# Performance work log

Measured on AMD Instinct MI355X. Metric: run time of the kernel, lower is better.

The kernel has to match this reference:

```python
import jax, jax.numpy as jnp
import numpy as np

D, R, C = 4, 6, 32
P = 2 * R + 1          # 13 (both pixel patch and memory patch, since memory_patch_R == R)
N = P * P              # 169
DIL_INT = 15


def corr_sampler(f1, f2, p, dil):
    """SpatialCorrelationSampler(kernel_size=1, patch_size=p, dilation_patch=dil).
    out[b,i,j,y,x] = sum_c f1[b,c,y,x] * f2[b,c, y+(i-Rp)*dil, x+(j-Rp)*dil] (zero pad)."""
    Rp = (p - 1) // 2
    pad = Rp * dil
    b, c, h, w = f1.shape
    f2p = jnp.pad(f2, ((0, 0), (0, 0), (pad, pad), (pad, pad)))
    outs = [jnp.einsum('bchw,bchw->bhw', f1, f2p[:, :, i * dil:i * dil + h, j * dil:j * dil + w])
            for i in range(p) for j in range(p)]
    return jnp.stack(outs, 1).reshape(b, p, p, h, w)


def bilinear_gather(im, ys, xs):
    """Bilinear sample im [b,c,H,W] at float coords ys,xs [b,N,h,w]; zeros outside."""
    H, W = im.shape[2], im.shape[3]
    y0 = jnp.floor(ys)
    x0 = jnp.floor(xs)
    wy = ys - y0
    wx = xs - x0

    def g(yi, xi):
        valid = ((yi >= 0) & (yi < H) & (xi >= 0) & (xi < W)).astype(im.dtype)
        yc = jnp.clip(yi, 0, H - 1).astype(jnp.int32)
        xc = jnp.clip(xi, 0, W - 1).astype(jnp.int32)
        out = jax.vmap(lambda imb, yb, xb: imb[:, yb, xb])(im, yc, xc)  # [b,c,N,h,w]
        return out * valid[:, None]

    return (g(y0, x0) * ((1 - wy) * (1 - wx))[:, None]
            + g(y0, x0 + 1) * ((1 - wy) * wx)[:, None]
            + g(y0 + 1, x0) * (wy * (1 - wx))[:, None]
            + g(y0 + 1, x0 + 1) * (wy * wx)[:, None])


def deform_im2col(im, offset, p):
    """Deformable im2col: for each output pixel (y,x) and kernel pos (ky,kx),
    bilinearly sample im at (y+ky-Rp+off_y, x+kx-Rp+off_x). offset [...,0]=x, [...,1]=y.
    Returns [b,c,p*p,h,w]."""
    b, c, h, w = im.shape
    Rp = (p - 1) // 2
    ky, kx = jnp.meshgrid(jnp.arange(p) - Rp, jnp.arange(p) - Rp, indexing='ij')
    ky = ky.reshape(-1).astype(im.dtype)
    kx = kx.reshape(-1).astype(im.dtype)
    ys = (jnp.arange(h, dtype=im.dtype)[None, None, :, None]
          + ky[None, :, None, None] + offset[..., 1][:, None])  # [b,N,h,w]
    xs = (jnp.arange(w, dtype=im.dtype)[None, None, None, :]
          + kx[None, :, None, None] + offset[..., 0][:, None])
    return bilinear_gather(im, ys, xs)


def unfold_patches(x, p, pad):
    """F.unfold(kernel_size=p, padding=pad) -> [b,c,p*p,h,w]."""
    b, c, h, w = x.shape
    xp = jnp.pad(x, ((0, 0), (0, 0), (pad, pad), (pad, pad)))
    cols = [xp[:, :, i:i + h, j:j + w] for i in range(p) for j in range(p)]
    return jnp.stack(cols, 2)


def _forward(feats_r, feats_t, quantized_r, ref_index, current_ind):
    ri = np.asarray(ref_index)
    ci = int(current_ind)
    diffs = [ci - int(x) for x in ri]
    nsearch = sum(1 for d in diffs if d > DIL_INT)
    dirates = [min(4, d // DIL_INT + 1) for d in diffs if d > DIL_INT]
    nref = feats_r.shape[0]
    b, c, h, w = feats_t.shape

    # offset grid: _y,_x = meshgrid(ij) so grid[...,0]=x-offset, grid[...,1]=y-offset
    _y, _x = jnp.meshgrid(jnp.arange(-R, R + 1), jnp.arange(-R, R + 1), indexing='ij')
    grid = jnp.stack([_x, _y], -1).astype(feats_t.dtype)  # [P,P,2]

    corrs_pixel = []
    offset0 = []
    for s in range(nsearch):
        cc = corr_sampler(feats_t, feats_r[s], P, dirates[s])             # [b,P,P,h,w]
        soft = jax.nn.softmax(cc.reshape(b, N, h * w), axis=1).reshape(b, P, P, h, w)
        off = jnp.einsum('bijhw,ijd->bhwd', soft, grid) * dirates[s]      # [b,h,w,2]
        offset0.append(off)
        col0 = deform_im2col(feats_r[s], off, P)                          # [b,c,N,h,w]
        corrs_pixel.append(jnp.einsum('bchw,bcnhw->bnhw', feats_t, col0).reshape(b, N, h * w))
    for ind in range(nsearch, nref):
        corrs_pixel.append(corr_sampler(feats_t, feats_r[ind], P, 1).reshape(b, N, h * w))

    corr_pixel = jax.nn.softmax(jnp.concatenate(corrs_pixel, 1), axis=1)  # [b,nref*N,h*w]

    # prep: float + stride-D subsampling (C-channel input, so no one-hot branch)
    qr = [quantized_r[i][:, :, ::D, ::D] for i in range(nref)]            # [b,C,h,w]
    cols = [deform_im2col(qr[i], offset0[i], P).reshape(b, C, N, h * w) for i in range(nsearch)]
    cols += [unfold_patches(qr[i], P, R).reshape(b, C, N, h * w) for i in range(nsearch, nref)]
    image_uf = jnp.concatenate(cols, 2)                                   # [b,C,nref*N,h*w]

    out = jnp.einsum('bkl,bckl->bcl', corr_pixel, image_uf).reshape(b, C, h, w)
    return out


def setup_inputs() -> dict:
    key = jax.random.key(0)
    k1, k2, k3 = jax.random.split(key, 3)
    feats_r = jax.random.normal(k1, (3, 1, 64, 56, 56), jnp.float32) * 0.2
    feats_t = jax.random.normal(k2, (1, 64, 56, 56), jnp.float32) * 0.2
    quantized_r = jax.random.uniform(k3, (3, 1, 32, 224, 224), jnp.float32)
    return {
        'feats_r': feats_r,
        'feats_t': feats_t,
        'quantized_r': quantized_r,
        'ref_index': np.array([0, 30, 39], dtype=np.int64),
        'current_ind': 40,
    }


def reference(feats_r, feats_t, quantized_r, ref_index, current_ind):
    return _forward(feats_r, feats_t, quantized_r, ref_index, current_ind)
```

## Files before the change

kernel.cpp:

```cpp
#include <hip/hip_runtime.h>

#define HW    56
#define NPIX  3136
#define CH    64
#define CQ    32
#define PS    13
#define NPOS  169
#define GS    14
#define NG    196
#define G1    15
#define NG1   225

typedef __attribute__((ext_vector_type(8))) short short8;
typedef __attribute__((ext_vector_type(8))) ushort ushort8;
typedef __attribute__((ext_vector_type(4))) float f32x4;

__device__ inline ushort f2bf(float f) {
  unsigned u = __float_as_uint(f);
  return (ushort)((u + 0x7fffu + ((u >> 16) & 1u)) >> 16);
}
__device__ inline float bf2f(ushort u) {
  return __uint_as_float((unsigned)u << 16);
}
__device__ inline void wave_sync() {
  asm volatile("s_waitcnt lgkmcnt(0)" ::: "memory");
  __builtin_amdgcn_sched_barrier(0);
}

__global__ __launch_bounds__(256) void prep_all(
    const float* __restrict__ ft_in,
    const float* __restrict__ fr_in,
    const float* __restrict__ q_in,
    ushort* __restrict__ ft_out,
    ushort* __restrict__ fr_out,
    ushort* __restrict__ qout,
    float* __restrict__ zrow) {
  __shared__ float smem[CQ * (HW + 1)];
  int bid = blockIdx.x, tid = threadIdx.x;
  if (bid < 784) {
    if (bid == 0 && tid < 64) zrow[tid] = 0.f;
    int m = bid / 196, t = bid - m * 196;
    int row0 = (t / 98) * 32;
    int col0 = (t - (t / 98) * 98) * 32;
    const float* src = (m == 0) ? ft_in : fr_in + (size_t)(m - 1) * CH * NPIX;
    ushort* dst      = (m == 0) ? ft_out : fr_out + (size_t)(m - 1) * NPIX * CH;
    int ty = tid >> 3, tx4 = (tid & 7) * 4;
    f32x4 v = *(const f32x4*)&src[(size_t)(row0 + ty) * NPIX + col0 + tx4];
    *(f32x4*)&smem[ty * 33 + tx4] = v;
    __syncthreads();
    int px = tid >> 3, c4 = (tid & 7) * 4;
    ushort4 o;
    o.x = f2bf(smem[(c4 + 0) * 33 + px]);
    o.y = f2bf(smem[(c4 + 1) * 33 + px]);
    o.z = f2bf(smem[(c4 + 2) * 33 + px]);
    o.w = f2bf(smem[(c4 + 3) * 33 + px]);
    *(ushort4*)&dst[(size_t)(col0 + px) * CH + row0 + c4] = o;
  } else {
    int q = bid - 784;
    int r = q / HW, yy = q - r * HW;
    for (int idx = tid; idx < CQ * HW; idx += 256) {
      int c = idx / HW, xx = idx - c * HW;
      smem[c * (HW + 1) + xx] = q_in[((size_t)(r * CQ + c) * 224 + yy * 4) * 224 + xx * 4];
    }
    __syncthreads();
    for (int idx = tid; idx < CQ * HW; idx += 256) {
      int xx = idx >> 5, c = idx & 31;
      qout[(size_t)r * NPIX * CQ + (size_t)(yy * HW + xx) * CQ + c] = f2bf(smem[c * (HW + 1) + xx]);
    }
  }
}

__global__ __launch_bounds__(256, 4) void colorizer_main(
    const ushort* __restrict__ ftb,
    const ushort* __restrict__ frb,
    const ushort* __restrict__ qrb,
    const ushort* __restrict__ zrow,
    float* __restrict__ out)
{
  __shared__ float C1[1024];
  __shared__ float C2[1024];
  __shared__ int   pw[4 * 832];
  __shared__ float s12w[16];
  __shared__ float Sas[4];
  __shared__ float fqr0[128];
  __shared__ float red2[512];

  int tid = threadIdx.x;
  int wid = tid >> 6, lane = tid & 63;
  int mrow = lane & 15, klane = lane >> 4;

  int bx = blockIdx.x % 28, by = blockIdx.x / 28;
  int Y0 = by * 2, X0 = bx * 2;
  int dy = wid >> 1, dx = wid & 1;
  int y = Y0 + dy, x = X0 + dx;
  int pix = y * HW + x;

  int*   wb   = pw + wid * 832;
  float* e    = (float*)wb;
  float* D    = (float*)(wb + 176);
  float* wg   = (float*)(wb + 384);
  int*   offg = wb + 608;
  float* cc   = (float*)offg;

  if (lane < 16) offg[208 + lane] = -1;

  const ushort* frb0 = frb;
  const ushort* frb1 = frb + (size_t)NPIX * CH;
  const ushort* frb2 = frb + (size_t)2 * NPIX * CH;
  const ushort* qr0b = qrb;
  const ushort* qr1b = qrb + (size_t)NPIX * CQ;
  const ushort* qr2b = qrb + (size_t)2 * NPIX * CQ;

  const ushort* fb = ftb + (size_t)pix * CH;
  const ushort* plo = (mrow == 0) ? (fb + klane * 8) : zrow;
  const ushort* phi = (mrow == 0) ? (fb + 32 + klane * 8) : zrow;
  short8 b_lo = *(const short8*)plo;
  short8 b_hi = *(const short8*)phi;

  const ushort* fb4 = (mrow < 4)
      ? (ftb + (size_t)((Y0 + (mrow >> 1)) * HW + X0 + (mrow & 1)) * CH)
      : zrow;
  short8 b4_lo = *(const short8*)(fb4 + klane * 8);
  short8 b4_hi = *(const short8*)(fb4 + 32 + klane * 8);

#pragma unroll
  for (int k = 0; k < 11; ++k) {
    if (k < 8) {
      int j = wid + 4 * k;
      if (j < 30) {
        int r = (j >= 15);
        int t = j - r * 15;
        int g = t * 16 + mrow;
        int gy = g / G1, gx = g - gy * G1;
        int sy = Y0 - 6 + gy, sx = X0 - 6 + gx;
        bool v = (g < NG1) && ((unsigned)sy < HW) && ((unsigned)sx < HW);
        const ushort* base = r ? frb2 : frb1;
        const ushort* rb = v ? (base + (size_t)(sy * HW + sx) * CH) : zrow;
        short8 alo = *(const short8*)(rb + klane * 8);
        short8 ahi = *(const short8*)(rb + 32 + klane * 8);
        f32x4 acc = {0.f, 0.f, 0.f, 0.f};
        acc = __builtin_amdgcn_mfma_f32_16x16x32_bf16(alo, b4_lo, acc, 0, 0, 0);
        acc = __builtin_amdgcn_mfma_f32_16x16x32_bf16(ahi, b4_hi, acc, 0, 0, 0);
        int col = lane & 15;
        if (col < 4) {
          float* Cd = r ? C2 : C1;
          int row0 = t * 16 + (lane >> 4) * 4;
#pragma unroll
          for (int q = 0; q < 4; ++q) Cd[(row0 + q) * 4 + col] = acc[q];
        }
      }
    }
    {
      int d = k * 16 + mrow;
      int ii = d / PS, jj = d - ii * PS;
      int sy = y + (ii - 6) * 3, sx = x + (jj - 6) * 3;
      bool v = (d < NPOS) && ((unsigned)sy < HW) && ((unsigned)sx < HW);
      const ushort* rb = v ? (frb0 + (size_t)(sy * HW + sx) * CH) : zrow;
      short8 alo = *(const short8*)(rb + klane * 8);
      short8 ahi = *(const short8*)(rb + 32 + klane * 8);
      f32x4 acc = {0.f, 0.f, 0.f, 0.f};
      acc = __builtin_amdgcn_mfma_f32_16x16x32_bf16(alo, b_lo, acc, 0, 0, 0);
      acc = __builtin_amdgcn_mfma_f32_16x16x32_bf16(ahi, b_hi, acc, 0, 0, 0);
      if (mrow == 0) *(f32x4*)&cc[k * 16 + klane * 4] = acc;
    }
  }
  __syncthreads();

  float sacc = 0.f;
#pragma unroll
  for (int t = 0; t < 8; ++t) {
    int idx = tid + t * 256;
    int ref = idx >> 10;
    int ix = idx & 1023;
    int g = ix >> 2, p = ix & 3;
    int gy = g / G1, gx = g - gy * G1;
    int ii = gy - (p >> 1), jj = gx - (p & 1);
    bool win = (g < NG1) && ((unsigned)ii < PS) && ((unsigned)jj < PS);
    float* Cd = ref ? C2 : C1;
    float val = Cd[ix];
    float ev = win ? __expf(val) : 0.f;
    Cd[ix] = ev;
    sacc += ev;
  }
#pragma unroll
  for (int o = 4; o <= 32; o <<= 1) sacc += __shfl_xor(sacc, o);
  if (lane < 4) s12w[wid * 4 + lane] = sacc;

  float se = 0.f, sxe = 0.f, sye = 0.f;
#pragma unroll
  for (int k = 0; k < 3; ++k) {
    int id = lane + 64 * k;
    if (id < NPOS) {
      float ex = __expf(cc[id]);
      int pi = id / PS, pj = id - (id / PS) * PS;
      se += ex;
      sxe += ex * (float)(pj - 6);
      sye += ex * (float)(pi - 6);
    }
  }
#pragma unroll
  for (int o = 1; o < 64; o <<= 1) {
    se  += __shfl_xor(se, o);
    sxe += __shfl_xor(sxe, o);
    sye += __shfl_xor(sye, o);
  }
  float offx = 3.f * sxe / se;
  float offy = 3.f * sye / se;

  float fy0 = floorf(offy), fx0 = floorf(offx);
  int   iy0 = (int)fy0,     ix0 = (int)fx0;
  float wyf = offy - fy0,   wxf = offx - fx0;
  float w00 = (1.f - wyf) * (1.f - wxf), w01 = (1.f - wyf) * wxf;
  float w10 = wyf * (1.f - wxf),         w11 = wyf * wxf;
  __syncthreads();

  {
    int q8 = tid & 7, s = tid >> 3;
    float a12[4][4];
#pragma unroll
    for (int p = 0; p < 4; ++p)
#pragma unroll
      for (int c = 0; c < 4; ++c) a12[p][c] = 0.f;
#pragma unroll
    for (int i = 0; i < 8; ++i) {
      int g = s + 32 * i;
      if (g < NG1) {
        int gy = g / G1, gx = g - gy * G1;
        int sy = Y0 - 6 + gy, sx = X0 - 6 + gx;
        if (((unsigned)sy < HW) && ((unsigned)sx < HW)) {
          size_t ro = (size_t)(sy * HW + sx) * CQ + q8 * 4;
          ushort4 u1 = *(const ushort4*)(qr1b + ro);
          ushort4 u2 = *(const ushort4*)(qr2b + ro);
          f32x4 w1 = *(f32x4*)&C1[g * 4];
          f32x4 w2 = *(f32x4*)&C2[g * 4];
          float q1[4] = {bf2f(u1.x), bf2f(u1.y), bf2f(u1.z), bf2f(u1.w)};
          float q2[4] = {bf2f(u2.x), bf2f(u2.y), bf2f(u2.z), bf2f(u2.w)};
#pragma unroll
          for (int p = 0; p < 4; ++p)
#pragma unroll
            for (int c = 0; c < 4; ++c)
              a12[p][c] += w1[p] * q1[c] + w2[p] * q2[c];
        }
      }
    }
#pragma unroll
    for (int o = 8; o <= 32; o <<= 1)
#pragma unroll
      for (int p = 0; p < 4; ++p)
#pragma unroll
        for (int c = 0; c < 4; ++c)
          a12[p][c] += __shfl_xor(a12[p][c], o);
    if (lane < 8) {
#pragma unroll
      for (int p = 0; p < 4; ++p)
#pragma unroll
        for (int c = 0; c < 4; ++c)
          red2[wid * 128 + lane * 16 + p * 4 + c] = a12[p][c];
    }
  }

#pragma unroll
  for (int g = 0; g < 13; ++g) {
    int d = g * 16 + mrow;
    int a = d / GS, bq = d - a * GS;
    int sy = y + iy0 + a - 6, sx = x + ix0 + bq - 6;
    bool vA = (d < NG) && ((unsigned)sy < HW) && ((unsigned)sx < HW);
    int roA = sy * HW + sx;
    const ushort* rbA = vA ? (frb0 + (size_t)roA * CH) : zrow;
    short8 aAlo = *(const short8*)(rbA + klane * 8);
    short8 aAhi = *(const short8*)(rbA + 32 + klane * 8);
    f32x4 accA = {0.f, 0.f, 0.f, 0.f};
    accA = __builtin_amdgcn_mfma_f32_16x16x32_bf16(aAlo, b_lo, accA, 0, 0, 0);
    accA = __builtin_amdgcn_mfma_f32_16x16x32_bf16(aAhi, b_hi, accA, 0, 0, 0);
    if (klane == 0) offg[d] = vA ? roA : -1;
    if (mrow == 0) *(f32x4*)&D[g * 16 + klane * 4] = accA;
  }
  wave_sync();

  float ps = 0.f;
#pragma unroll
  for (int k = 0; k < 3; ++k) {
    int id = lane + 64 * k;
    if (id < NPOS) {
      int pi = id / PS, pj = id - (id / PS) * PS;
      float c0 = w00 * D[pi * GS + pj]       + w01 * D[pi * GS + pj + 1]
               + w10 * D[(pi + 1) * GS + pj] + w11 * D[(pi + 1) * GS + pj + 1];
      float ex = __expf(c0);
      e[id] = ex;
      ps += ex;
    } else if (id < 176) {
      e[id] = 0.f;
    }
  }
#pragma unroll
  for (int o = 1; o < 64; o <<= 1) ps += __shfl_xor(ps, o);
  if (lane == 0)
    Sas[wid] = ps + s12w[wid] + s12w[4 + wid] + s12w[8 + wid] + s12w[12 + wid];
  wave_sync();

#pragma unroll
  for (int k = 0; k < 4; ++k) {
    int t = lane + 64 * k;
    if (t < 224) {
      float acc = 0.f;
      if (t < NG) {
        int a = t / GS, bq2 = t - (t / GS) * GS;
        if (a < PS && bq2 < PS) acc += w00 * e[a * PS + bq2];
        if (a < PS && bq2 >= 1) acc += w01 * e[a * PS + bq2 - 1];
        if (a >= 1 && bq2 < PS) acc += w10 * e[(a - 1) * PS + bq2];
        if (a >= 1 && bq2 >= 1) acc += w11 * e[(a - 1) * PS + bq2 - 1];
      }
      wg[t] = acc;
    }
  }
  wave_sync();

  int slot = lane >> 2, ln4 = lane & 3;
  float acc8[8];
#pragma unroll
  for (int c = 0; c < 8; ++c) acc8[c] = 0.f;
#pragma unroll
  for (int k = 0; k < 14; ++k) {
    int d = slot + k * 16;
    int ro = offg[d];
    if (ro >= 0) {
      float w = wg[d];
      ushort8 u = *(const ushort8*)(qr0b + (size_t)ro * CQ + ln4 * 8);
#pragma unroll
      for (int c = 0; c < 8; ++c) acc8[c] = fmaf(w, bf2f(u[c]), acc8[c]);
    }
  }
#pragma unroll
  for (int o = 4; o <= 32; o <<= 1)
#pragma unroll
    for (int c = 0; c < 8; ++c) acc8[c] += __shfl_xor(acc8[c], o);
  if (lane < 4) {
#pragma unroll
    for (int c = 0; c < 8; ++c) fqr0[wid * 32 + lane * 8 + c] = acc8[c];
  }
  __syncthreads();

  if (tid < 128) {
    int p = tid >> 5, c = tid & 31;
    float tot = fqr0[p * 32 + c];
#pragma unroll
    for (int w = 0; w < 4; ++w)
      tot += red2[w * 128 + (c >> 2) * 16 + p * 4 + (c & 3)];
    int pidx = (Y0 + (p >> 1)) * HW + X0 + (p & 1);
    out[(size_t)c * NPIX + pidx] = tot / Sas[p];
  }
}

extern "C" void kernel_launch(void* const* d_in, const int* in_sizes, int n_in,
                              void* d_out, int out_size, void* d_ws, size_t ws_size,
                              hipStream_t stream) {
  const float* feats_r     = (const float*)d_in[0];
  const float* feats_t     = (const float*)d_in[1];
  const float* quantized_r = (const float*)d_in[2];

  ushort* ftb = (ushort*)d_ws;
  ushort* frb = ftb + 200704;
  ushort* qrb = frb + 602112;
  float*  zro = (float*)(qrb + 301056);

  prep_all<<<952, 256, 0, stream>>>(feats_t, feats_r, quantized_r,
                                    ftb, frb, qrb, zro);
  colorizer_main<<<784, 256, 0, stream>>>(ftb, frb, qrb, (const ushort*)zro,
                                          (float*)d_out);
}
```

Baseline: 42.90 us.

## Batch global loads ahead of MFMA and FMA loops to raise memory-level parallelism

Splits each gather+MFMA loop into a phase that issues all global loads into register arrays, then a compute phase, so many loads are in flight at once instead of serialized behind conditionals. Out-of-range loads are redirected to a zero row to make them unconditional. The launch bound drops from 4 to 3 blocks per CU to allow the larger register footprint, trading occupancy for per-wave latency hiding.

After: 43.87 us. 2.3% more time.

```diff
diff --git a/kernel.cpp b/kernel.cpp
--- a/kernel.cpp
+++ b/kernel.cpp
@@ -70,7 +70,7 @@
   }
 }
 
-__global__ __launch_bounds__(256, 4) void colorizer_main(
+__global__ __launch_bounds__(256, 3) void colorizer_main(
     const ushort* __restrict__ ftb,
     const ushort* __restrict__ frb,
     const ushort* __restrict__ qrb,
@@ -123,45 +123,60 @@
   short8 b4_lo = *(const short8*)(fb4 + klane * 8);
   short8 b4_hi = *(const short8*)(fb4 + 32 + klane * 8);
 
-#pragma unroll
-  for (int k = 0; k < 11; ++k) {
-    if (k < 8) {
-      int j = wid + 4 * k;
-      if (j < 30) {
-        int r = (j >= 15);
-        int t = j - r * 15;
-        int g = t * 16 + mrow;
-        int gy = g / G1, gx = g - gy * G1;
-        int sy = Y0 - 6 + gy, sx = X0 - 6 + gx;
-        bool v = (g < NG1) && ((unsigned)sy < HW) && ((unsigned)sx < HW);
-        const ushort* base = r ? frb2 : frb1;
-        const ushort* rb = v ? (base + (size_t)(sy * HW + sx) * CH) : zrow;
-        short8 alo = *(const short8*)(rb + klane * 8);
-        short8 ahi = *(const short8*)(rb + 32 + klane * 8);
-        f32x4 acc = {0.f, 0.f, 0.f, 0.f};
-        acc = __builtin_amdgcn_mfma_f32_16x16x32_bf16(alo, b4_lo, acc, 0, 0, 0);
-        acc = __builtin_amdgcn_mfma_f32_16x16x32_bf16(ahi, b4_hi, acc, 0, 0, 0);
-        int col = lane & 15;
-        if (col < 4) {
-          float* Cd = r ? C2 : C1;
-          int row0 = t * 16 + (lane >> 4) * 4;
-#pragma unroll
-          for (int q = 0; q < 4; ++q) Cd[(row0 + q) * 4 + col] = acc[q];
-        }
-      }
-    }
-    {
+  {
+    short8 a0[11][2];
+#pragma unroll
+    for (int k = 0; k < 11; ++k) {
       int d = k * 16 + mrow;
       int ii = d / PS, jj = d - ii * PS;
       int sy = y + (ii - 6) * 3, sx = x + (jj - 6) * 3;
       bool v = (d < NPOS) && ((unsigned)sy < HW) && ((unsigned)sx < HW);
       const ushort* rb = v ? (frb0 + (size_t)(sy * HW + sx) * CH) : zrow;
-      short8 alo = *(const short8*)(rb + klane * 8);
-      short8 ahi = *(const short8*)(rb + 32 + klane * 8);
+      a0[k][0] = *(const short8*)(rb + klane * 8);
+      a0[k][1] = *(const short8*)(rb + 32 + klane * 8);
+    }
+#pragma unroll
+    for (int k = 0; k < 11; ++k) {
       f32x4 acc = {0.f, 0.f, 0.f, 0.f};
-      acc = __builtin_amdgcn_mfma_f32_16x16x32_bf16(alo, b_lo, acc, 0, 0, 0);
-      acc = __builtin_amdgcn_mfma_f32_16x16x32_bf16(ahi, b_hi, acc, 0, 0, 0);
+      acc = __builtin_amdgcn_mfma_f32_16x16x32_bf16(a0[k][0], b_lo, acc, 0, 0, 0);
+      acc = __builtin_amdgcn_mfma_f32_16x16x32_bf16(a0[k][1], b_hi, acc, 0, 0, 0);
       if (mrow == 0) *(f32x4*)&cc[k * 16 + klane * 4] = acc;
+    }
+  }
+
+  {
+    short8 a1[8][2];
+#pragma unroll
+    for (int k = 0; k < 8; ++k) {
+      int j = wid + 4 * k;
+      int r = (j >= 15);
+      int t = j - r * 15;
+      int g = t * 16 + mrow;
+      int gy = g / G1, gx = g - gy * G1;
+      int sy = Y0 - 6 + gy, sx = X0 - 6 + gx;
+      bool v = (j < 30) && (g < NG1) && ((unsigned)sy < HW) && ((unsigned)sx < HW);
+      const ushort* base = r ? frb2 : frb1;
+      const ushort* rb = v ? (base + (size_t)(sy * HW + sx) * CH) : zrow;
+      a1[k][0] = *(const short8*)(rb + klane * 8);
+      a1[k][1] = *(const short8*)(rb + 32 + klane * 8);
+    }
+#pragma unroll
+    for (int k = 0; k < 8; ++k) {
+      int j = wid + 4 * k;
+      if (j < 30) {
+        int r = (j >= 15);
+        int t = j - r * 15;
+        f32x4 acc = {0.f, 0.f, 0.f, 0.f};
+        acc = __builtin_amdgcn_mfma_f32_16x16x32_bf16(a1[k][0], b4_lo, acc, 0, 0, 0);
+        acc = __builtin_amdgcn_mfma_f32_16x16x32_bf16(a1[k][1], b4_hi, acc, 0, 0, 0);
+        int col = lane & 15;
+        if (col < 4) {
+          float* Cd = r ? C2 : C1;
+          int row0 = t * 16 + (lane >> 4) * 4;
+#pragma unroll
+          for (int q = 0; q < 4; ++q) Cd[(row0 + q) * 4 + col] = acc[q];
+        }
+      }
     }
   }
   __syncthreads();
@@ -216,6 +231,19 @@
 
   {
     int q8 = tid & 7, s = tid >> 3;
+    ushort4 qu1[8], qu2[8];
+#pragma unroll
+    for (int i = 0; i < 8; ++i) {
+      int g = s + 32 * i;
+      int gy = g / G1, gx = g - gy * G1;
+      int sy = Y0 - 6 + gy, sx = X0 - 6 + gx;
+      bool v = (g < NG1) && ((unsigned)sy < HW) && ((unsigned)sx < HW);
+      size_t ro = (size_t)(sy * HW + sx) * CQ + q8 * 4;
+      const ushort* p1 = v ? (qr1b + ro) : zrow;
+      const ushort* p2 = v ? (qr2b + ro) : zrow;
+      qu1[i] = *(const ushort4*)p1;
+      qu2[i] = *(const ushort4*)p2;
+    }
     float a12[4][4];
 #pragma unroll
     for (int p = 0; p < 4; ++p)
@@ -225,22 +253,15 @@
     for (int i = 0; i < 8; ++i) {
       int g = s + 32 * i;
       if (g < NG1) {
-        int gy = g / G1, gx = g - gy * G1;
-        int sy = Y0 - 6 + gy, sx = X0 - 6 + gx;
-        if (((unsigned)sy < HW) && ((unsigned)sx < HW)) {
-          size_t ro = (size_t)(sy * HW + sx) * CQ + q8 * 4;
-          ushort4 u1 = *(const ushort4*)(qr1b + ro);
-          ushort4 u2 = *(const ushort4*)(qr2b + ro);
-          f32x4 w1 = *(f32x4*)&C1[g * 4];
-          f32x4 w2 = *(f32x4*)&C2[g * 4];
-          float q1[4] = {bf2f(u1.x), bf2f(u1.y), bf2f(u1.z), bf2f(u1.w)};
-          float q2[4] = {bf2f(u2.x), bf2f(u2.y), bf2f(u2.z), bf2f(u2.w)};
-#pragma unroll
-          for (int p = 0; p < 4; ++p)
-#pragma unroll
-            for (int c = 0; c < 4; ++c)
-              a12[p][c] += w1[p] * q1[c] + w2[p] * q2[c];
-        }
+        f32x4 w1 = *(f32x4*)&C1[g * 4];
+        f32x4 w2 = *(f32x4*)&C2[g * 4];
+        float q1[4] = {bf2f(qu1[i].x), bf2f(qu1[i].y), bf2f(qu1[i].z), bf2f(qu1[i].w)};
+        float q2[4] = {bf2f(qu2[i].x), bf2f(qu2[i].y), bf2f(qu2[i].z), bf2f(qu2[i].w)};
+#pragma unroll
+        for (int p = 0; p < 4; ++p)
+#pragma unroll
+          for (int c = 0; c < 4; ++c)
+            a12[p][c] += w1[p] * q1[c] + w2[p] * q2[c];
       }
     }
 #pragma unroll
@@ -259,21 +280,27 @@
     }
   }
 
-#pragma unroll
-  for (int g = 0; g < 13; ++g) {
-    int d = g * 16 + mrow;
-    int a = d / GS, bq = d - a * GS;
-    int sy = y + iy0 + a - 6, sx = x + ix0 + bq - 6;
-    bool vA = (d < NG) && ((unsigned)sy < HW) && ((unsigned)sx < HW);
-    int roA = sy * HW + sx;
-    const ushort* rbA = vA ? (frb0 + (size_t)roA * CH) : zrow;
-    short8 aAlo = *(const short8*)(rbA + klane * 8);
-    short8 aAhi = *(const short8*)(rbA + 32 + klane * 8);
-    f32x4 accA = {0.f, 0.f, 0.f, 0.f};
-    accA = __builtin_amdgcn_mfma_f32_16x16x32_bf16(aAlo, b_lo, accA, 0, 0, 0);
-    accA = __builtin_amdgcn_mfma_f32_16x16x32_bf16(aAhi, b_hi, accA, 0, 0, 0);
-    if (klane == 0) offg[d] = vA ? roA : -1;
-    if (mrow == 0) *(f32x4*)&D[g * 16 + klane * 4] = accA;
+  {
+    short8 a2[13][2];
+#pragma unroll
+    for (int g = 0; g < 13; ++g) {
+      int d = g * 16 + mrow;
+      int a = d / GS, bq = d - a * GS;
+      int sy = y + iy0 + a - 6, sx = x + ix0 + bq - 6;
+      bool vA = (d < NG) && ((unsigned)sy < HW) && ((unsigned)sx < HW);
+      int roA = sy * HW + sx;
+      const ushort* rbA = vA ? (frb0 + (size_t)roA * CH) : zrow;
+      a2[g][0] = *(const short8*)(rbA + klane * 8);
+      a2[g][1] = *(const short8*)(rbA + 32 + klane * 8);
+      if (klane == 0) offg[d] = vA ? roA : -1;
+    }
+#pragma unroll
+    for (int g = 0; g < 13; ++g) {
+      f32x4 accA = {0.f, 0.f, 0.f, 0.f};
+      accA = __builtin_amdgcn_mfma_f32_16x16x32_bf16(a2[g][0], b_lo, accA, 0, 0, 0);
+      accA = __builtin_amdgcn_mfma_f32_16x16x32_bf16(a2[g][1], b_hi, accA, 0, 0, 0);
+      if (mrow == 0) *(f32x4*)&D[g * 16 + klane * 4] = accA;
+    }
   }
   wave_sync();
 
@@ -315,28 +342,34 @@
   }
   wave_sync();
 
-  int slot = lane >> 2, ln4 = lane & 3;
-  float acc8[8];
-#pragma unroll
-  for (int c = 0; c < 8; ++c) acc8[c] = 0.f;
-#pragma unroll
-  for (int k = 0; k < 14; ++k) {
-    int d = slot + k * 16;
-    int ro = offg[d];
-    if (ro >= 0) {
-      float w = wg[d];
-      ushort8 u = *(const ushort8*)(qr0b + (size_t)ro * CQ + ln4 * 8);
-#pragma unroll
-      for (int c = 0; c < 8; ++c) acc8[c] = fmaf(w, bf2f(u[c]), acc8[c]);
-    }
-  }
-#pragma unroll
-  for (int o = 4; o <= 32; o <<= 1)
-#pragma unroll
-    for (int c = 0; c < 8; ++c) acc8[c] += __shfl_xor(acc8[c], o);
-  if (lane < 4) {
-#pragma unroll
-    for (int c = 0; c < 8; ++c) fqr0[wid * 32 + lane * 8 + c] = acc8[c];
+  {
+    int slot = lane >> 2, ln4 = lane & 3;
+    ushort8 qv[14];
+    float wv[14];
+#pragma unroll
+    for (int k = 0; k < 14; ++k) {
+      int d = slot + k * 16;
+      int ro = offg[d];
+      wv[k] = wg[d];
+      const ushort* p = (ro >= 0) ? (qr0b + (size_t)ro * CQ + ln4 * 8) : zrow;
+      qv[k] = *(const ushort8*)p;
+    }
+    float acc8[8];
+#pragma unroll
+    for (int c = 0; c < 8; ++c) acc8[c] = 0.f;
+#pragma unroll
+    for (int k = 0; k < 14; ++k) {
+#pragma unroll
+      for (int c = 0; c < 8; ++c) acc8[c] = fmaf(wv[k], bf2f(qv[k][c]), acc8[c]);
+    }
+#pragma unroll
+    for (int o = 4; o <= 32; o <<= 1)
+#pragma unroll
+      for (int c = 0; c < 8; ++c) acc8[c] += __shfl_xor(acc8[c], o);
+    if (lane < 4) {
+#pragma unroll
+      for (int c = 0; c < 8; ++c) fqr0[wid * 32 + lane * 8 + c] = acc8[c];
+    }
   }
   __syncthreads();
 
```
